# Kernel tuning notes

Hardware: AMD Instinct MI355X
Metric: run time of the kernel (lower is better)

The kernel has to match this reference:

```python
import jax, jax.numpy as jnp
import numpy as np

N = 50000
D = 64
E = 600000
NNZ = 800000


def setup_inputs() -> dict:
    key = jax.random.key(0)
    ks = jax.random.split(key, 12)
    s = 1.0 / np.sqrt(D)
    return {
        "emb": jax.random.normal(ks[0], (N, D), jnp.float32) * s,
        "W1": jax.random.normal(ks[1], (D, 2 * D), jnp.float32) * s,
        "b1": jnp.zeros((2 * D,), jnp.float32),
        "W2": jax.random.normal(ks[2], (2 * D, D), jnp.float32) * (1.0 / np.sqrt(2 * D)),
        "b2": jnp.zeros((D,), jnp.float32),
        "gamma": jnp.ones((D,), jnp.float32),
        "beta": jnp.zeros((D,), jnp.float32),
        "hgc1_bias": jnp.zeros((D,), jnp.float32),
        "fc1_W": jax.random.normal(ks[3], (D, D), jnp.float32) * s,
        "fus_l1_W": jax.random.normal(ks[4], (D, D), jnp.float32) * s,
        "fus_l1_b": jnp.zeros((D,), jnp.float32),
        "fus_l2_W": jax.random.normal(ks[5], (1, D), jnp.float32) * s,
        "fus_l2_b": jnp.zeros((1,), jnp.float32),
        "hg_val": jax.random.uniform(ks[6], (NNZ,), jnp.float32) * 0.05,
        "edge_index": jax.random.randint(ks[7], (2, E), 0, N, jnp.int32),
        "hg_row": jax.random.randint(ks[8], (NNZ,), 0, N, jnp.int32),
        "hg_col": jax.random.randint(ks[9], (NNZ,), 0, N, jnp.int32),
    }


def gcn_conv(x, W, b, src, dst):
    # PyG-style GCNConv: add self loops, sym-normalized aggregation of x@W
    loop = jnp.arange(N, dtype=src.dtype)
    s = jnp.concatenate([src, loop])
    t = jnp.concatenate([dst, loop])
    deg = jax.ops.segment_sum(jnp.ones_like(t, jnp.float32), t, num_segments=N)
    dinv = jax.lax.rsqrt(jnp.maximum(deg, 1.0))
    norm = dinv[s] * dinv[t]                       # [E+N]
    xw = x @ W                                     # [N, out]
    msg = norm[:, None] * xw[s]                    # gather (irregular)
    return jax.ops.segment_sum(msg, t, num_segments=N) + b


def reference(emb, W1, b1, W2, b2, gamma, beta, hgc1_bias, fc1_W,
              fus_l1_W, fus_l1_b, fus_l2_W, fus_l2_b, hg_val,
              edge_index, hg_row, hg_col):
    src, dst = edge_index[0], edge_index[1]
    # ---- GraphNN: two GCN layers + BatchNorm (batch stats, eval dropout) ----
    h1 = gcn_conv(emb, W1, b1, src, dst)           # [N, 2D]
    h2 = gcn_conv(h1, W2, b2, src, dst)            # [N, D]
    mu = jnp.mean(h2, axis=0)
    var = jnp.var(h2, axis=0)
    hidden = (h2 - mu) * jax.lax.rsqrt(var + 1e-5) * gamma + beta
    # ---- HGNN2 / HGNN_conv: edge = G.T@x ; x = G@edge (sparse matmuls) ----
    x = jax.nn.relu(hidden) + hgc1_bias
    edge_emb = jax.ops.segment_sum(hg_val[:, None] * x[hg_row], hg_col, num_segments=N)
    x = jax.ops.segment_sum(hg_val[:, None] * edge_emb[hg_col], hg_row, num_segments=N)
    x = jax.nn.softmax(x, axis=1)
    sub_node = x @ fc1_W.T                         # fc1 (no bias)
    # ---- Fusion gate over {hidden, sub_node} ----
    stacked = jnp.stack([hidden, sub_node], axis=0)          # [2, N, D]
    g = jnp.tanh(stacked @ fus_l1_W.T + fus_l1_b)
    score = jax.nn.softmax(g @ fus_l2_W.T + fus_l2_b, axis=0)  # [2, N, 1]
    out = jnp.sum(score * stacked, axis=0)                   # [N, D]
    return out
```

## Files before the change

kernel.cpp:

```cpp
#include <hip/hip_runtime.h>
#include <hip/hip_fp16.h>


#define SEGSH 8
#define MAXSEG 256
#define PBLK 256

__global__ __launch_bounds__(256) void p1_count_kernel(const int* __restrict__ dst, int e,
                                                       const int* __restrict__ row,
                                                       const int* __restrict__ col, int nnz,
                                                       int* __restrict__ blockcnt, int nseg) {
    __shared__ int lc[3 * MAXSEG];
    for (int i = threadIdx.x; i < 3 * nseg; i += 256) lc[i] = 0;
    __syncthreads();
    int ce = (e + PBLK - 1) / PBLK;
    int cz = (nnz + PBLK - 1) / PBLK;
    int e0 = blockIdx.x * ce, e1 = min(e0 + ce, e);
    for (int i = e0 + threadIdx.x; i < e1; i += 256)
        atomicAdd(&lc[dst[i] >> SEGSH], 1);
    int z0 = blockIdx.x * cz, z1 = min(z0 + cz, nnz);
    for (int i = z0 + threadIdx.x; i < z1; i += 256) {
        atomicAdd(&lc[nseg + (col[i] >> SEGSH)], 1);
        atomicAdd(&lc[2 * nseg + (row[i] >> SEGSH)], 1);
    }
    __syncthreads();
    for (int r = threadIdx.x; r < 3 * nseg; r += 256)
        blockcnt[r * PBLK + blockIdx.x] = lc[r];
}

__global__ __launch_bounds__(256) void p2a_kernel(int* __restrict__ blockcnt,
                                                  int* __restrict__ segtot, int rows) {
    int rw = blockIdx.x * 4 + (threadIdx.x >> 6);
    if (rw >= rows) return;
    int ln = threadIdx.x & 63;
    int b = rw * PBLK + ln * 4;
    int v0 = blockcnt[b], v1 = blockcnt[b + 1], v2 = blockcnt[b + 2], v3 = blockcnt[b + 3];
    int s = v0 + v1 + v2 + v3;
    int incl = s;
    for (int d = 1; d < 64; d <<= 1) {
        int t = __shfl_up(incl, d, 64);
        if (ln >= d) incl += t;
    }
    int excl = incl - s;
    blockcnt[b]     = excl;
    blockcnt[b + 1] = excl + v0;
    blockcnt[b + 2] = excl + v0 + v1;
    blockcnt[b + 3] = excl + v0 + v1 + v2;
    if (ln == 63) segtot[rw] = incl;
}

__global__ __launch_bounds__(192) void p2b_kernel(const int* __restrict__ segtot,
                                                  int* __restrict__ segoff, int nseg) {
    int st = threadIdx.x >> 6, ln = threadIdx.x & 63;
    int chunk = (nseg + 63) / 64;
    int s0 = ln * chunk, s1 = min(s0 + chunk, nseg);
    int sum = 0;
    for (int i = s0; i < s1; ++i) sum += segtot[st * nseg + i];
    int incl = sum;
    for (int d = 1; d < 64; d <<= 1) {
        int v = __shfl_up(incl, d, 64);
        if (ln >= d) incl += v;
    }
    int run = incl - sum;
    for (int i = s0; i < s1; ++i) {
        segoff[st * nseg + i] = run;
        run += segtot[st * nseg + i];
    }
}

__global__ __launch_bounds__(256) void p3_scatter_kernel(const int* __restrict__ src,
                                                         const int* __restrict__ dst, int e,
                                                         const int* __restrict__ row,
                                                         const int* __restrict__ col,
                                                         const float* __restrict__ val, int nnz,
                                                         const int* __restrict__ blockcnt,
                                                         const int* __restrict__ segoff,
                                                         unsigned* __restrict__ runG,
                                                         uint2* __restrict__ runC,
                                                         uint2* __restrict__ runR, int nseg) {
    __shared__ int base[3 * MAXSEG];
    __shared__ int cnt[3 * MAXSEG];
    for (int i = threadIdx.x; i < 3 * nseg; i += 256) {
        base[i] = segoff[i] + blockcnt[i * PBLK + blockIdx.x];
        cnt[i] = 0;
    }
    __syncthreads();
    int ce = (e + PBLK - 1) / PBLK;
    int cz = (nnz + PBLK - 1) / PBLK;
    int e0 = blockIdx.x * ce, e1 = min(e0 + ce, e);
    for (int i = e0 + threadIdx.x; i < e1; i += 256) {
        int d = dst[i];
        int sg = d >> SEGSH;
        int p = atomicAdd(&cnt[sg], 1);
        runG[base[sg] + p] = ((unsigned)d << 16) | (unsigned)src[i];
    }
    int z0 = blockIdx.x * cz, z1 = min(z0 + cz, nnz);
    for (int i = z0 + threadIdx.x; i < z1; i += 256) {
        int r = row[i], c = col[i];
        unsigned hv = (unsigned)__half_as_ushort(__float2half(val[i]));
        int sgc = nseg + (c >> SEGSH);
        int p = atomicAdd(&cnt[sgc], 1);
        runC[base[sgc] + p] = make_uint2((unsigned)c, ((unsigned)r << 16) | hv);
        int sgr = 2 * nseg + (r >> SEGSH);
        p = atomicAdd(&cnt[sgr], 1);
        runR[base[sgr] + p] = make_uint2((unsigned)r, ((unsigned)c << 16) | hv);
    }
}

__global__ __launch_bounds__(256) void csr_build_kernel(const unsigned* __restrict__ runG,
                                                        const uint2* __restrict__ runC,
                                                        const uint2* __restrict__ runR,
                                                        const int* __restrict__ segoff,
                                                        const int* __restrict__ segtot,
                                                        int nseg, int n,
                                                        int* __restrict__ gcn_off,
                                                        int* __restrict__ hgc_off,
                                                        int* __restrict__ hgr_off,
                                                        float* __restrict__ dinv,
                                                        unsigned short* __restrict__ gsrcs,
                                                        unsigned* __restrict__ entc,
                                                        unsigned* __restrict__ entr) {
    __shared__ int cG[256], cC[256], cR[256];
    int s = blockIdx.x;
    int t = threadIdx.x;
    cG[t] = 0; cC[t] = 0; cR[t] = 0;
    __syncthreads();
    int oG = segoff[s],            nG = segtot[s];
    int oC = segoff[nseg + s],     nC = segtot[nseg + s];
    int oR = segoff[2 * nseg + s], nR = segtot[2 * nseg + s];
    for (int i = t; i < nG; i += 256) atomicAdd(&cG[(runG[oG + i] >> 16) & 255], 1);
    for (int i = t; i < nC; i += 256) atomicAdd(&cC[runC[oC + i].x & 255], 1);
    for (int i = t; i < nR; i += 256) atomicAdd(&cR[runR[oR + i].x & 255], 1);
    __syncthreads();
    int vG = cG[t], vC = cC[t], vR = cR[t];
    for (int d = 1; d < 256; d <<= 1) {
        int tG = (t >= d) ? cG[t - d] : 0;
        int tC = (t >= d) ? cC[t - d] : 0;
        int tR = (t >= d) ? cR[t - d] : 0;
        __syncthreads();
        cG[t] += tG; cC[t] += tC; cR[t] += tR;
        __syncthreads();
    }
    int eG = cG[t] - vG, eC = cC[t] - vC, eR = cR[t] - vR;
    int key = (s << SEGSH) + t;
    if (key < n) {
        gcn_off[key] = oG + eG;
        hgc_off[key] = oC + eC;
        hgr_off[key] = oR + eR;
        dinv[key] = rsqrtf((float)(vG + 1));
    }
    if (key == n) {
        gcn_off[n] = oG + eG;
        hgc_off[n] = oC + eC;
        hgr_off[n] = oR + eR;
    }
    if (s == nseg - 1 && t == 255 && ((n & 255) == 0)) {
        gcn_off[n] = oG + cG[255];
        hgc_off[n] = oC + cC[255];
        hgr_off[n] = oR + cR[255];
    }
    __syncthreads();
    cG[t] = oG + eG; cC[t] = oC + eC; cR[t] = oR + eR;
    __syncthreads();
    for (int i = t; i < nG; i += 256) {
        unsigned u = runG[oG + i];
        int p = atomicAdd(&cG[(u >> 16) & 255], 1);
        gsrcs[p] = (unsigned short)(u & 0xffffu);
    }
    for (int i = t; i < nC; i += 256) {
        uint2 u = runC[oC + i];
        int p = atomicAdd(&cC[u.x & 255], 1);
        entc[p] = u.y;
    }
    for (int i = t; i < nR; i += 256) {
        uint2 u = runR[oR + i];
        int p = atomicAdd(&cR[u.x & 255], 1);
        entr[p] = u.y;
    }
}

__global__ __launch_bounds__(64) void wprep_kernel(const float* __restrict__ W1,
                                                   const float* __restrict__ W2,
                                                   const float* __restrict__ b1,
                                                   float* __restrict__ W12,
                                                   float* __restrict__ bw) {
    int r = blockIdx.x;
    int c = threadIdx.x;
    const float* a = (r < 64) ? (W1 + r * 128) : b1;
    float acc = 0.f;
#pragma unroll 8
    for (int k = 0; k < 128; ++k) acc = fmaf(a[k], W2[k * 64 + c], acc);
    if (r < 64) W12[r * 64 + c] = acc;
    else bw[c] = acc;
}

template <bool SDI>
__global__ __launch_bounds__(256) void gcn_gather_kernel(const float* __restrict__ x,
                                                         const float* __restrict__ dinv,
                                                         const int* __restrict__ off,
                                                         const unsigned short* __restrict__ srcs,
                                                         float* __restrict__ out,
                                                         float* __restrict__ sdi, int n) {
    int node = blockIdx.x * 4 + (threadIdx.x >> 6);
    if (node >= n) return;
    int lane = threadIdx.x & 63;
    int sub = lane >> 4;
    int q = lane & 15;
    int e0 = off[node], e1 = off[node + 1];
    float4 acc = make_float4(0.f, 0.f, 0.f, 0.f);
    float dsum = 0.f;
    int e = e0 + sub;
    int s = (e < e1) ? (int)srcs[e] : 0;
    float ds = (e < e1) ? dinv[s] : 0.f;
    for (; e < e1; e += 4) {
        int sn = (e + 4 < e1) ? (int)srcs[e + 4] : 0;
        float dsn = (e + 4 < e1) ? dinv[sn] : 0.f;
        const float4 v = *(const float4*)(x + (long long)s * 64 + q * 4);
        acc.x = fmaf(ds, v.x, acc.x);
        acc.y = fmaf(ds, v.y, acc.y);
        acc.z = fmaf(ds, v.z, acc.z);
        acc.w = fmaf(ds, v.w, acc.w);
        dsum += ds;
        s = sn; ds = dsn;
    }
    acc.x += __shfl_xor(acc.x, 16, 64); acc.x += __shfl_xor(acc.x, 32, 64);
    acc.y += __shfl_xor(acc.y, 16, 64); acc.y += __shfl_xor(acc.y, 32, 64);
    acc.z += __shfl_xor(acc.z, 16, 64); acc.z += __shfl_xor(acc.z, 32, 64);
    acc.w += __shfl_xor(acc.w, 16, 64); acc.w += __shfl_xor(acc.w, 32, 64);
    if (SDI) { dsum += __shfl_xor(dsum, 16, 64); dsum += __shfl_xor(dsum, 32, 64); }
    if (sub == 0) {
        float dt = dinv[node];
        const float4 xs = *(const float4*)(x + (long long)node * 64 + q * 4);
        float4 o;
        o.x = dt * fmaf(dt, xs.x, acc.x);
        o.y = dt * fmaf(dt, xs.y, acc.y);
        o.z = dt * fmaf(dt, xs.z, acc.z);
        o.w = dt * fmaf(dt, xs.w, acc.w);
        *(float4*)(out + (long long)node * 64 + q * 4) = o;
        if (SDI && q == 0) sdi[node] = dt * (dt + dsum);
    }
}

__global__ __launch_bounds__(256) void gemm_h2_kernel(const float* __restrict__ X,
                                                      const float* __restrict__ W12,
                                                      const float* __restrict__ bw,
                                                      const float* __restrict__ b2,
                                                      const float* __restrict__ sdi,
                                                      float* __restrict__ h2,
                                                      float* __restrict__ stats, int n) {
    __shared__ float Wl[64 * 64];
    __shared__ float cadd[64], b2l[64];
    __shared__ float ls[4][64], ls2[4][64];
    for (int i = threadIdx.x; i < 4096; i += 256) Wl[i] = W12[i];
    if (threadIdx.x < 64) cadd[threadIdx.x] = bw[threadIdx.x];
    else if (threadIdx.x < 128) b2l[threadIdx.x - 64] = b2[threadIdx.x - 64];
    __syncthreads();
    int m = threadIdx.x & 63;
    int g = threadIdx.x >> 6;
    float sl = 0.f, s2l = 0.f;
    int rend = (blockIdx.x + 1) * 32; if (rend > n) rend = n;
    for (int r = blockIdx.x * 32 + g; r < rend; r += 4) {
        const float* xr = X + (long long)r * 64;
        float acc = 0.0f;
#pragma unroll 8
        for (int k = 0; k < 64; ++k) acc = fmaf(xr[k], Wl[k * 64 + m], acc);
        float v = acc + sdi[r] * cadd[m] + b2l[m];
        h2[(long long)r * 64 + m] = v;
        sl += v; s2l += v * v;
    }
    ls[g][m] = sl; ls2[g][m] = s2l;
    __syncthreads();
    if (g == 0) {
        float s  = ls[0][m] + ls[1][m] + ls[2][m] + ls[3][m];
        float s2 = ls2[0][m] + ls2[1][m] + ls2[2][m] + ls2[3][m];
        atomicAdd(&stats[m], s);
        atomicAdd(&stats[64 + m], s2);
    }
}

template <bool BN>
__global__ __launch_bounds__(256) void hg_gather_kernel(const float* __restrict__ in,
                                                        const int* __restrict__ off,
                                                        const unsigned* __restrict__ ents,
                                                        const float* __restrict__ stats,
                                                        const float* __restrict__ gamma,
                                                        const float* __restrict__ beta,
                                                        const float* __restrict__ hbias,
                                                        float invN,
                                                        float* __restrict__ out, int n) {
    int node = blockIdx.x * 4 + (threadIdx.x >> 6);
    if (node >= n) return;
    int lane = threadIdx.x & 63;
    int sub = lane >> 4;
    int q = lane & 15;
    float sc[4], sh[4], hb[4];
    if (BN) {
#pragma unroll
        for (int c = 0; c < 4; ++c) {
            int col = q * 4 + c;
            float mu = stats[col] * invN;
            float var = stats[64 + col] * invN - mu * mu;
            float s = gamma[col] * rsqrtf(var + 1e-5f);
            sc[c] = s; sh[c] = beta[col] - mu * s; hb[c] = hbias[col];
        }
    }
    int e0 = off[node], e1 = off[node + 1];
    float4 acc = make_float4(0.f, 0.f, 0.f, 0.f);
    int e = e0 + sub;
    unsigned t = (e < e1) ? ents[e] : 0u;
    for (; e < e1; e += 4) {
        unsigned tn = (e + 4 < e1) ? ents[e + 4] : 0u;
        float vv = __half2float(__ushort_as_half((unsigned short)(t & 0xffffu)));
        float4 v = *(const float4*)(in + (long long)(t >> 16) * 64 + q * 4);
        if (BN) {
            v.x = fmaxf(fmaf(v.x, sc[0], sh[0]), 0.f) + hb[0];
            v.y = fmaxf(fmaf(v.y, sc[1], sh[1]), 0.f) + hb[1];
            v.z = fmaxf(fmaf(v.z, sc[2], sh[2]), 0.f) + hb[2];
            v.w = fmaxf(fmaf(v.w, sc[3], sh[3]), 0.f) + hb[3];
        }
        acc.x = fmaf(vv, v.x, acc.x);
        acc.y = fmaf(vv, v.y, acc.y);
        acc.z = fmaf(vv, v.z, acc.z);
        acc.w = fmaf(vv, v.w, acc.w);
        t = tn;
    }
    acc.x += __shfl_xor(acc.x, 16, 64); acc.x += __shfl_xor(acc.x, 32, 64);
    acc.y += __shfl_xor(acc.y, 16, 64); acc.y += __shfl_xor(acc.y, 32, 64);
    acc.z += __shfl_xor(acc.z, 16, 64); acc.z += __shfl_xor(acc.z, 32, 64);
    acc.w += __shfl_xor(acc.w, 16, 64); acc.w += __shfl_xor(acc.w, 32, 64);
    if (sub == 0) *(float4*)(out + (long long)node * 64 + q * 4) = acc;
}

#define TPAD 68
__device__ __forceinline__ float dot4(float4 a, float4 b) {
    return fmaf(a.x, b.x, fmaf(a.y, b.y, fmaf(a.z, b.z, a.w * b.w)));
}

__global__ __launch_bounds__(256) void tail_kernel(const float* __restrict__ x2,
                                                   const float* __restrict__ h2raw,
                                                   const float* __restrict__ fc1_W,
                                                   const float* __restrict__ fusW1,
                                                   const float* __restrict__ b1,
                                                   const float* __restrict__ w2,
                                                   const float* __restrict__ b2,
                                                   const float* __restrict__ stats,
                                                   const float* __restrict__ gamma,
                                                   const float* __restrict__ beta,
                                                   float invN,
                                                   float* __restrict__ out, int n) {
    __shared__ float A[64 * TPAD];
    __shared__ float Hs[64 * TPAD];
    __shared__ float WL[64 * TPAD];
    __shared__ float bsc[64], bsh[64];
    int t = threadIdx.x;
    int tx = t & 15, ty = t >> 4;
    int r0 = blockIdx.x * 64;

    if (t < 64) {
        float mu = stats[t] * invN;
        float var = stats[64 + t] * invN - mu * mu;
        float s = gamma[t] * rsqrtf(var + 1e-5f);
        bsc[t] = s; bsh[t] = beta[t] - mu * s;
    }
    __syncthreads();

    float b1d[4], w2d[4];
#pragma unroll
    for (int di = 0; di < 4; ++di) {
        b1d[di] = b1[tx + 16 * di];
        w2d[di] = w2[tx + 16 * di];
    }
    float b20 = b2[0];

    for (int f = t; f < 1024; f += 256) {
        int d = f >> 4, k4 = (f & 15) << 2;
        *(float4*)&WL[d * TPAD + k4] = *(const float4*)&fc1_W[d * 64 + k4];
        int gr = r0 + d;
        float4 hv = make_float4(0.f, 0.f, 0.f, 0.f);
        if (gr < n) {
            hv = *(const float4*)&h2raw[(long long)gr * 64 + k4];
            hv.x = fmaf(hv.x, bsc[k4],     bsh[k4]);
            hv.y = fmaf(hv.y, bsc[k4 + 1], bsh[k4 + 1]);
            hv.z = fmaf(hv.z, bsc[k4 + 2], bsh[k4 + 2]);
            hv.w = fmaf(hv.w, bsc[k4 + 3], bsh[k4 + 3]);
        }
        *(float4*)&Hs[d * TPAD + k4] = hv;
    }

#pragma unroll
    for (int ri = 0; ri < 4; ++ri) {
        int rl = 4 * ty + ri;
        int r = r0 + rl;
        bool ok = r < n;
        float vv[4];
#pragma unroll
        for (int di = 0; di < 4; ++di)
            vv[di] = ok ? x2[(long long)r * 64 + tx + 16 * di] : 0.f;
        float m = fmaxf(fmaxf(vv[0], vv[1]), fmaxf(vv[2], vv[3]));
        for (int s = 1; s < 16; s <<= 1) m = fmaxf(m, __shfl_xor(m, s, 16));
        float e0 = expf(vv[0] - m), e1 = expf(vv[1] - m);
        float e2 = expf(vv[2] - m), e3 = expf(vv[3] - m);
        float sm = e0 + e1 + e2 + e3;
        for (int s = 1; s < 16; s <<= 1) sm += __shfl_xor(sm, s, 16);
        float inv = 1.0f / sm;
        A[rl * TPAD + tx]      = e0 * inv;
        A[rl * TPAD + tx + 16] = e1 * inv;
        A[rl * TPAD + tx + 32] = e2 * inv;
        A[rl * TPAD + tx + 48] = e3 * inv;
    }
    __syncthreads();

    float sn[4][4];
#pragma unroll
    for (int ri = 0; ri < 4; ++ri)
#pragma unroll
        for (int di = 0; di < 4; ++di) sn[ri][di] = 0.f;
    for (int k = 0; k < 64; k += 4) {
        float4 p4[4], w4[4];
#pragma unroll
        for (int ri = 0; ri < 4; ++ri) p4[ri] = *(float4*)&A[(4 * ty + ri) * TPAD + k];
#pragma unroll
        for (int di = 0; di < 4; ++di) w4[di] = *(float4*)&WL[(tx + 16 * di) * TPAD + k];
#pragma unroll
        for (int ri = 0; ri < 4; ++ri)
#pragma unroll
            for (int di = 0; di < 4; ++di)
                sn[ri][di] += dot4(p4[ri], w4[di]);
    }
    __syncthreads();

#pragma unroll
    for (int ri = 0; ri < 4; ++ri)
#pragma unroll
        for (int di = 0; di < 4; ++di)
            A[(4 * ty + ri) * TPAD + tx + 16 * di] = sn[ri][di];
    for (int f = t; f < 1024; f += 256) {
        int d = f >> 4, k4 = (f & 15) << 2;
        *(float4*)&WL[d * TPAD + k4] = *(const float4*)&fusW1[d * 64 + k4];
    }
    __syncthreads();

    float aH[4][4], aS[4][4];
#pragma unroll
    for (int ri = 0; ri < 4; ++ri)
#pragma unroll
        for (int di = 0; di < 4; ++di) { aH[ri][di] = b1d[di]; aS[ri][di] = b1d[di]; }
    for (int k = 0; k < 64; k += 4) {
        float4 h4[4], s4[4], w4[4];
#pragma unroll
        for (int ri = 0; ri < 4; ++ri) {
            h4[ri] = *(float4*)&Hs[(4 * ty + ri) * TPAD + k];
            s4[ri] = *(float4*)&A[(4 * ty + ri) * TPAD + k];
        }
#pragma unroll
        for (int di = 0; di < 4; ++di) w4[di] = *(float4*)&WL[(tx + 16 * di) * TPAD + k];
#pragma unroll
        for (int ri = 0; ri < 4; ++ri)
#pragma unroll
            for (int di = 0; di < 4; ++di) {
                aH[ri][di] += dot4(h4[ri], w4[di]);
                aS[ri][di] += dot4(s4[ri], w4[di]);
            }
    }

#pragma unroll
    for (int ri = 0; ri < 4; ++ri) {
        int rl = 4 * ty + ri;
        int r = r0 + rl;
        float pH = 0.f, pS = 0.f;
#pragma unroll
        for (int di = 0; di < 4; ++di) {
            pH = fmaf(tanhf(aH[ri][di]), w2d[di], pH);
            pS = fmaf(tanhf(aS[ri][di]), w2d[di], pS);
        }
        for (int s = 1; s < 16; s <<= 1) {
            pH += __shfl_xor(pH, s, 16);
            pS += __shfl_xor(pS, s, 16);
        }
        pH += b20; pS += b20;
        float mx = fmaxf(pH, pS);
        float eH = expf(pH - mx), eS = expf(pS - mx);
        float inv = 1.0f / (eH + eS);
        if (r < n) {
#pragma unroll
            for (int di = 0; di < 4; ++di) {
                int d = tx + 16 * di;
                float hv = Hs[rl * TPAD + d];
                out[(long long)r * 64 + d] = (eH * hv + eS * sn[ri][di]) * inv;
            }
        }
    }
}

extern "C" void kernel_launch(void* const* d_in, const int* in_sizes, int n_in,
                              void* d_out, int out_size, void* d_ws, size_t ws_size,
                              hipStream_t stream) {
    const float* emb       = (const float*)d_in[0];
    const float* W1        = (const float*)d_in[1];
    const float* b1        = (const float*)d_in[2];
    const float* W2        = (const float*)d_in[3];
    const float* b2        = (const float*)d_in[4];
    const float* gamma     = (const float*)d_in[5];
    const float* beta      = (const float*)d_in[6];
    const float* hgc1_bias = (const float*)d_in[7];
    const float* fc1_W     = (const float*)d_in[8];
    const float* fus_l1_W  = (const float*)d_in[9];
    const float* fus_l1_b  = (const float*)d_in[10];
    const float* fus_l2_W  = (const float*)d_in[11];
    const float* fus_l2_b  = (const float*)d_in[12];
    const float* hg_val    = (const float*)d_in[13];
    const int*   edge_index= (const int*)d_in[14];
    const int*   hg_row    = (const int*)d_in[15];
    const int*   hg_col    = (const int*)d_in[16];

    const int N    = in_sizes[0] / 64;
    const int E    = in_sizes[14] / 2;
    const int NNZ  = in_sizes[13];
    const int Np   = (N + 3) & ~3;
    const int NSEG = (N + 255) >> 8;
    const int* src = edge_index;
    const int* dst = edge_index + E;

    float* ws      = (float*)d_ws;
    float* dinv    = ws;
    float* sdi     = dinv + Np;
    float* w12     = sdi + Np;
    float* bw      = w12 + 4096;
    float* stats   = bw + 64;
    int*   gcn_off = (int*)(stats + 128);
    int*   hgc_off = gcn_off + (Np + 4);
    int*   hgr_off = hgc_off + (Np + 4);
    int*   segtot  = hgr_off + (Np + 4);
    int*   segoff  = segtot + 3 * NSEG;
    int*   blockcnt= segoff + 3 * NSEG;
    unsigned short* gcn_srcs = (unsigned short*)(blockcnt + 3 * NSEG * PBLK);
    unsigned* hgc_ent = (unsigned*)(gcn_srcs + ((E + 1) & ~1));
    unsigned* hgr_ent = hgc_ent + NNZ;
    float* buf1    = (float*)(hgr_ent + NNZ);
    float* buf2    = buf1 + (size_t)128 * Np;

    const int Ep = (E + 1) & ~1;
    unsigned* runG = (unsigned*)buf1;
    uint2*    runC = (uint2*)(runG + Ep);
    uint2*    runR = runC + NNZ;

    float* tbuf = buf2;
    float* ubuf = buf1;
    float* h2   = buf1 + (size_t)64 * Np;
    float* eemb = buf2;
    float* x2   = buf1;
    float* out  = (float*)d_out;

    const float invN = 1.0f / (float)N;

    hipMemsetAsync(stats, 0, 128 * sizeof(float), stream);
    p1_count_kernel<<<PBLK, 256, 0, stream>>>(dst, E, hg_row, hg_col, NNZ, blockcnt, NSEG);
    p2a_kernel<<<(3 * NSEG + 3) / 4, 256, 0, stream>>>(blockcnt, segtot, 3 * NSEG);
    p2b_kernel<<<1, 192, 0, stream>>>(segtot, segoff, NSEG);
    p3_scatter_kernel<<<PBLK, 256, 0, stream>>>(src, dst, E, hg_row, hg_col, hg_val, NNZ,
                                                blockcnt, segoff, runG, runC, runR, NSEG);
    csr_build_kernel<<<NSEG, 256, 0, stream>>>(runG, runC, runR, segoff, segtot, NSEG, N,
                                               gcn_off, hgc_off, hgr_off, dinv,
                                               gcn_srcs, hgc_ent, hgr_ent);

    wprep_kernel<<<65, 64, 0, stream>>>(W1, W2, b1, w12, bw);
    gcn_gather_kernel<true><<<(N + 3) / 4, 256, 0, stream>>>(emb, dinv, gcn_off, gcn_srcs,
                                                             tbuf, sdi, N);
    gcn_gather_kernel<false><<<(N + 3) / 4, 256, 0, stream>>>(tbuf, dinv, gcn_off, gcn_srcs,
                                                              ubuf, nullptr, N);
    gemm_h2_kernel<<<(N + 31) / 32, 256, 0, stream>>>(ubuf, w12, bw, b2, sdi, h2, stats, N);

    hg_gather_kernel<true><<<(N + 3) / 4, 256, 0, stream>>>(h2, hgc_off, hgc_ent,
                                                            stats, gamma, beta, hgc1_bias,
                                                            invN, eemb, N);
    hg_gather_kernel<false><<<(N + 3) / 4, 256, 0, stream>>>(eemb, hgr_off, hgr_ent,
                                                             nullptr, nullptr, nullptr, nullptr,
                                                             0.f, x2, N);

    tail_kernel<<<(N + 63) / 64, 256, 0, stream>>>(x2, h2, fc1_W, fus_l1_W, fus_l1_b,
                                                   fus_l2_W, fus_l2_b, stats, gamma, beta,
                                                   invN, out, N);
}
```

Before: 319.6 us.

## Register-tile the h2 GEMM with shared-memory X and W tiles

```diff
diff --git a/kernel.cpp b/kernel.cpp
--- a/kernel.cpp
+++ b/kernel.cpp
@@ -241,6 +241,7 @@
     }
 }
 
+#define GP 68
 __global__ __launch_bounds__(256) void gemm_h2_kernel(const float* __restrict__ X,
                                                       const float* __restrict__ W12,
                                                       const float* __restrict__ bw,
@@ -248,33 +249,78 @@
                                                       const float* __restrict__ sdi,
                                                       float* __restrict__ h2,
                                                       float* __restrict__ stats, int n) {
-    __shared__ float Wl[64 * 64];
+    __shared__ float Xs[64 * GP];
+    __shared__ float WL[64 * GP];
     __shared__ float cadd[64], b2l[64];
-    __shared__ float ls[4][64], ls2[4][64];
-    for (int i = threadIdx.x; i < 4096; i += 256) Wl[i] = W12[i];
-    if (threadIdx.x < 64) cadd[threadIdx.x] = bw[threadIdx.x];
-    else if (threadIdx.x < 128) b2l[threadIdx.x - 64] = b2[threadIdx.x - 64];
-    __syncthreads();
-    int m = threadIdx.x & 63;
-    int g = threadIdx.x >> 6;
-    float sl = 0.f, s2l = 0.f;
-    int rend = (blockIdx.x + 1) * 32; if (rend > n) rend = n;
-    for (int r = blockIdx.x * 32 + g; r < rend; r += 4) {
-        const float* xr = X + (long long)r * 64;
-        float acc = 0.0f;
-#pragma unroll 8
-        for (int k = 0; k < 64; ++k) acc = fmaf(xr[k], Wl[k * 64 + m], acc);
-        float v = acc + sdi[r] * cadd[m] + b2l[m];
-        h2[(long long)r * 64 + m] = v;
-        sl += v; s2l += v * v;
-    }
-    ls[g][m] = sl; ls2[g][m] = s2l;
-    __syncthreads();
-    if (g == 0) {
-        float s  = ls[0][m] + ls[1][m] + ls[2][m] + ls[3][m];
-        float s2 = ls2[0][m] + ls2[1][m] + ls2[2][m] + ls2[3][m];
-        atomicAdd(&stats[m], s);
-        atomicAdd(&stats[64 + m], s2);
+    int t = threadIdx.x;
+    int tx = t & 15, ty = t >> 4;
+    int r0 = blockIdx.x * 64;
+    if (t < 64) cadd[t] = bw[t];
+    else if (t < 128) b2l[t - 64] = b2[t - 64];
+    for (int f = t; f < 1024; f += 256) {
+        int d = f >> 4, k4 = (f & 15) << 2;
+        *(float4*)&WL[d * GP + k4] = *(const float4*)&W12[d * 64 + k4];
+        int gr = r0 + d;
+        float4 xv = make_float4(0.f, 0.f, 0.f, 0.f);
+        if (gr < n) xv = *(const float4*)&X[(long long)gr * 64 + k4];
+        *(float4*)&Xs[d * GP + k4] = xv;
+    }
+    __syncthreads();
+
+    float4 acc[4];
+#pragma unroll
+    for (int ri = 0; ri < 4; ++ri) acc[ri] = make_float4(0.f, 0.f, 0.f, 0.f);
+    for (int k = 0; k < 64; k += 4) {
+        float4 w0 = *(float4*)&WL[(k + 0) * GP + 4 * tx];
+        float4 w1 = *(float4*)&WL[(k + 1) * GP + 4 * tx];
+        float4 w2v = *(float4*)&WL[(k + 2) * GP + 4 * tx];
+        float4 w3 = *(float4*)&WL[(k + 3) * GP + 4 * tx];
+#pragma unroll
+        for (int ri = 0; ri < 4; ++ri) {
+            float4 xv = *(float4*)&Xs[(4 * ty + ri) * GP + k];
+            acc[ri].x = fmaf(xv.x, w0.x, fmaf(xv.y, w1.x, fmaf(xv.z, w2v.x, fmaf(xv.w, w3.x, acc[ri].x))));
+            acc[ri].y = fmaf(xv.x, w0.y, fmaf(xv.y, w1.y, fmaf(xv.z, w2v.y, fmaf(xv.w, w3.y, acc[ri].y))));
+            acc[ri].z = fmaf(xv.x, w0.z, fmaf(xv.y, w1.z, fmaf(xv.z, w2v.z, fmaf(xv.w, w3.z, acc[ri].z))));
+            acc[ri].w = fmaf(xv.x, w0.w, fmaf(xv.y, w1.w, fmaf(xv.z, w2v.w, fmaf(xv.w, w3.w, acc[ri].w))));
+        }
+    }
+
+    float ps[4] = {0.f, 0.f, 0.f, 0.f}, pq[4] = {0.f, 0.f, 0.f, 0.f};
+    float ca[4] = {cadd[4 * tx], cadd[4 * tx + 1], cadd[4 * tx + 2], cadd[4 * tx + 3]};
+    float bb[4] = {b2l[4 * tx], b2l[4 * tx + 1], b2l[4 * tx + 2], b2l[4 * tx + 3]};
+#pragma unroll
+    for (int ri = 0; ri < 4; ++ri) {
+        int r = r0 + 4 * ty + ri;
+        if (r < n) {
+            float sd = sdi[r];
+            float4 v;
+            v.x = acc[ri].x + sd * ca[0] + bb[0];
+            v.y = acc[ri].y + sd * ca[1] + bb[1];
+            v.z = acc[ri].z + sd * ca[2] + bb[2];
+            v.w = acc[ri].w + sd * ca[3] + bb[3];
+            *(float4*)&h2[(long long)r * 64 + 4 * tx] = v;
+            ps[0] += v.x; ps[1] += v.y; ps[2] += v.z; ps[3] += v.w;
+            pq[0] += v.x * v.x; pq[1] += v.y * v.y; pq[2] += v.z * v.z; pq[3] += v.w * v.w;
+        }
+    }
+    __syncthreads();
+    float* lsum = Xs;
+    float* lsq  = Xs + 1024;
+#pragma unroll
+    for (int di = 0; di < 4; ++di) {
+        lsum[ty * 64 + 4 * tx + di] = ps[di];
+        lsq[ty * 64 + 4 * tx + di]  = pq[di];
+    }
+    __syncthreads();
+    if (t < 64) {
+        float s = 0.f, s2 = 0.f;
+#pragma unroll
+        for (int g = 0; g < 16; ++g) {
+            s += lsum[g * 64 + t];
+            s2 += lsq[g * 64 + t];
+        }
+        atomicAdd(&stats[t], s);
+        atomicAdd(&stats[64 + t], s2);
     }
 }
 
@@ -568,7 +614,7 @@
                                                              tbuf, sdi, N);
     gcn_gather_kernel<false><<<(N + 3) / 4, 256, 0, stream>>>(tbuf, dinv, gcn_off, gcn_srcs,
                                                               ubuf, nullptr, N);
-    gemm_h2_kernel<<<(N + 31) / 32, 256, 0, stream>>>(ubuf, w12, bw, b2, sdi, h2, stats, N);
+    gemm_h2_kernel<<<(N + 63) / 64, 256, 0, stream>>>(ubuf, w12, bw, b2, sdi, h2, stats, N);
 
     hg_gather_kernel<true><<<(N + 3) / 4, 256, 0, stream>>>(h2, hgc_off, hgc_ent,
                                                             stats, gamma, beta, hgc1_bias,
```

Result: faster. 292.8 us (-8.4%).
